# Performance work log

Hardware: AMD Instinct MI355X
Metric: run time of the kernel (lower is better)

Reference implementation:

```python
import jax, jax.numpy as jnp
import numpy as np

K = 512   # per-head dim == input dim
H = 8     # heads

def setup_inputs() -> dict:
    key = jax.random.key(0)
    ks = jax.random.split(key, 6)
    b, t = 4, 2048
    x = jax.random.normal(ks[0], (b, t, K), dtype=jnp.float32)
    s = 0.02
    Wq = jax.random.normal(ks[1], (K, K * H), dtype=jnp.float32) * s
    Wk = jax.random.normal(ks[2], (K, K * H), dtype=jnp.float32) * s
    Wv = jax.random.normal(ks[3], (K, K * H), dtype=jnp.float32) * s
    Wo = jax.random.normal(ks[4], (K * H, K), dtype=jnp.float32) * s
    bo = jnp.zeros((K,), dtype=jnp.float32)
    return {"x": x, "Wq": Wq, "Wk": Wk, "Wv": Wv, "Wo": Wo, "bo": bo}

def reference(x, Wq, Wk, Wv, Wo, bo):
    b, t, _ = x.shape
    scale = K ** 0.25
    # rearrange 'b t (k h) -> (b h) t k' == reshape (b,t,K,H) then move h next to b
    def split_heads(y):
        return y.reshape(b, t, K, H).transpose(0, 3, 1, 2)  # [b,h,t,K]
    q = split_heads(x @ Wq) / scale
    k_ = split_heads(x @ Wk) / scale
    v = split_heads(x @ Wv)
    dot = jnp.einsum('bhtk,bhsk->bhts', q, k_)      # [b,h,t,t]
    attn = jax.nn.softmax(dot, axis=-1)
    o = jnp.einsum('bhts,bhsk->bhtk', attn, v)      # [b,h,t,K]
    # '(b h) t k -> b t (h k)': heads outer in concat
    o = o.transpose(0, 2, 1, 3).reshape(b, t, H * K)
    return o @ Wo + bo
```

## Files before the change

kernel.cpp:

```cpp
#include <hip/hip_runtime.h>

typedef unsigned short u16;
typedef unsigned char u8;
typedef unsigned int u32;
typedef long i64;
typedef __attribute__((ext_vector_type(8))) short bf16x8;
typedef __attribute__((ext_vector_type(4))) float f32x4;
typedef __attribute__((ext_vector_type(16))) float f32x16;
typedef __attribute__((ext_vector_type(4))) u16 u16x4;
typedef __attribute__((ext_vector_type(4))) u32 u32x4;

__device__ __forceinline__ u16 f2bf(float f) {
  u32 u = __builtin_bit_cast(u32, f);
  return (u16)((u + 0x7FFFu + ((u >> 16) & 1u)) >> 16);
}
__device__ __forceinline__ u8 f2fp8(float f) {
  int w = __builtin_amdgcn_cvt_pk_fp8_f32(f, 0.f, 0, false);
  return (u8)(w & 0xff);
}

__device__ __forceinline__ f32x4 mfma16(bf16x8 a, bf16x8 b, f32x4 c) {
  return __builtin_amdgcn_mfma_f32_16x16x32_bf16(a, b, c, 0, 0, 0);
}
__device__ __forceinline__ f32x16 mfma32(bf16x8 a, bf16x8 b, f32x16 c) {
  return __builtin_amdgcn_mfma_f32_32x32x16_bf16(a, b, c, 0, 0, 0);
}
__device__ __forceinline__ f32x16 mfma32f8(i64 a, i64 b, f32x16 c) {
  return __builtin_amdgcn_mfma_f32_32x32x16_fp8_fp8(a, b, c, 0, 0, 0);
}

__device__ __forceinline__ void gload16(const void* g, void* l) {
  __builtin_amdgcn_global_load_lds(
      (const __attribute__((address_space(1))) unsigned int*)g,
      (__attribute__((address_space(3))) unsigned int*)l, 16, 0, 0);
}

__device__ __forceinline__ u32 cvtpk(float lo, float hi) {
  u32 r;
  asm volatile("v_cvt_pk_bf16_f32 %0, %1, %2" : "=v"(r) : "v"(lo), "v"(hi));
  return r;
}
__device__ __forceinline__ void pl32swap(u32& a, u32& b) {
  asm volatile("v_permlane32_swap_b32 %0, %1" : "+v"(a), "+v"(b));
}


__global__ void pack_x_kernel(const float* __restrict__ x, u16* __restrict__ xb) {
  const int i = blockIdx.x * 256 + threadIdx.x;
  const float4 v = ((const float4*)x)[i];
  u16x4 o;
  o[0] = f2bf(v.x); o[1] = f2bf(v.y); o[2] = f2bf(v.z); o[3] = f2bf(v.w);
  ((u16x4*)xb)[i] = o;
}

__global__ void pack_wqkv_t(const float* __restrict__ W, u16* __restrict__ Wp) {
  __shared__ u16 tile[64][72];
  const int t = threadIdx.x;
  const int c0 = blockIdx.x * 64, dd0 = blockIdx.y * 64;
#pragma unroll
  for (int s = 0; s < 4; ++s) {
    const int r = s * 16 + (t >> 4);
    const int q = (t & 15) * 4;
    const float4 v = *(const float4*)&W[(size_t)(dd0 + r) * 4096 + c0 + q];
    tile[r][q + 0] = f2bf(v.x); tile[r][q + 1] = f2bf(v.y);
    tile[r][q + 2] = f2bf(v.z); tile[r][q + 3] = f2bf(v.w);
  }
  __syncthreads();
#pragma unroll
  for (int s = 0; s < 4; ++s) {
    const int cl = s * 16 + (t >> 4);
    const int u = t & 15;
    const int cg = c0 + cl;
    const int orow = (cg & 7) * 512 + (cg >> 3);
    u16x4 o;
#pragma unroll
    for (int i = 0; i < 4; ++i) o[i] = tile[u * 4 + i][cl];
    *(u16x4*)&Wp[(size_t)orow * 512 + dd0 + u * 4] = o;
  }
}

__global__ void pack_wo_t(const float* __restrict__ W, u16* __restrict__ Wp) {
  __shared__ u16 tile[64][72];
  const int t = threadIdx.x;
  const int k0 = blockIdx.x * 64, n0 = blockIdx.y * 64;
#pragma unroll
  for (int s = 0; s < 4; ++s) {
    const int r = s * 16 + (t >> 4);
    const int q = (t & 15) * 4;
    const float4 v = *(const float4*)&W[(size_t)(k0 + r) * 512 + n0 + q];
    tile[r][q + 0] = f2bf(v.x); tile[r][q + 1] = f2bf(v.y);
    tile[r][q + 2] = f2bf(v.z); tile[r][q + 3] = f2bf(v.w);
  }
  __syncthreads();
#pragma unroll
  for (int s = 0; s < 4; ++s) {
    const int cl = s * 16 + (t >> 4);
    const int u = t & 15;
    u16x4 o;
#pragma unroll
    for (int i = 0; i < 4; ++i) o[i] = tile[u * 4 + i][cl];
    *(u16x4*)&Wp[(size_t)(n0 + cl) * 4096 + k0 + u * 4] = o;
  }
}


template <int MODE>
__global__ __launch_bounds__(256, 2) void gemm_bf16(
    const u16* __restrict__ A, const u16* __restrict__ B,
    void* __restrict__ Cout, const float* __restrict__ bias,
    int Kd, float scale) {
  __shared__ u16 Al[128 * 64];
  __shared__ u16 Bl[128 * 64];
  const int tid = threadIdx.x;
  const int lane = tid & 63;
  const int w = tid >> 6, wm = w >> 1, wn = w & 1;
  const int l15 = lane & 15, lg = lane >> 4;
  const int m0 = blockIdx.y * 128, n0 = blockIdx.x * 128;

  f32x4 acc[4][4];
  const f32x4 zero = {0.f, 0.f, 0.f, 0.f};
#pragma unroll
  for (int i = 0; i < 4; ++i)
#pragma unroll
    for (int j = 0; j < 4; ++j) acc[i][j] = zero;

  const int nk = Kd >> 6;
  for (int kt = 0; kt < nk; ++kt) {
    __syncthreads();
    const int k0 = kt << 6;
#pragma unroll
    for (int s = 0; s < 4; ++s) {
      const int chunk = s * 256 + tid;
      const int row = chunk >> 3, c = chunk & 7;
      const int cs = c ^ (row & 7);
      gload16(A + (size_t)(m0 + row) * Kd + k0 + cs * 8, &Al[chunk * 8]);
    }
#pragma unroll
    for (int s = 0; s < 4; ++s) {
      const int chunk = s * 256 + tid;
      const int row = chunk >> 3, c = chunk & 7;
      const int cs = c ^ (row & 7);
      gload16(B + (size_t)(n0 + row) * Kd + k0 + cs * 8, &Bl[chunk * 8]);
    }
    __syncthreads();
#pragma unroll
    for (int kk = 0; kk < 2; ++kk) {
      bf16x8 af[4], bfr[4];
      const int ch = kk * 4 + lg;
#pragma unroll
      for (int i = 0; i < 4; ++i) {
        const int ar = wm * 64 + i * 16 + l15;
        af[i] = *(const bf16x8*)&Al[ar * 64 + ((ch ^ (ar & 7)) * 8)];
        const int br = wn * 64 + i * 16 + l15;
        bfr[i] = *(const bf16x8*)&Bl[br * 64 + ((ch ^ (br & 7)) * 8)];
      }
#pragma unroll
      for (int i = 0; i < 4; ++i)
#pragma unroll
        for (int j = 0; j < 4; ++j)
          acc[i][j] = mfma16(af[i], bfr[j], acc[i][j]);
    }
  }

#pragma unroll
  for (int i = 0; i < 4; ++i) {
    const int gr0 = m0 + wm * 64 + i * 16 + lg * 4;
#pragma unroll
    for (int j = 0; j < 4; ++j) {
      const int gc = n0 + wn * 64 + j * 16 + l15;
      if constexpr (MODE == 0) {
        u8* O = (u8*)Cout;
        const int h = gc >> 9, d = gc & 511;
#pragma unroll
        for (int r = 0; r < 4; ++r) {
          const int grr = gr0 + r;
          const int bb = grr >> 11, t = grr & 2047;
          O[((size_t)((bb * 8 + h) * 2048 + t) << 9) + d] = f2fp8(acc[i][j][r] * scale);
        }
      } else if constexpr (MODE == 1) {
        u16* O = (u16*)Cout;
        const int h = gc >> 9, d = gc & 511;
        const int bb = gr0 >> 11, t = gr0 & 2047;
        u16x4 pk;
#pragma unroll
        for (int r = 0; r < 4; ++r) pk[r] = f2bf(acc[i][j][r]);
        *(u16x4*)&O[((size_t)((bb * 8 + h) * 512 + d) << 11) + t] = pk;
      } else if constexpr (MODE == 3) {
        u8* O = (u8*)Cout;
        const int h = gc >> 9, k = gc & 511;
#pragma unroll
        for (int r = 0; r < 4; ++r) {
          const int grr = gr0 + r;
          const int bb = grr >> 11, t = grr & 2047;
          O[((((size_t)(bb * 8 + h) * 64 + (t >> 5)) * 32 + (k >> 4)) * 32 + (t & 31)) * 16 +
            (k & 15)] = f2fp8(acc[i][j][r] * scale);
        }
      } else {
        float* O = (float*)Cout;
        const float bv = bias[gc];
#pragma unroll
        for (int r = 0; r < 4; ++r)
          O[(size_t)(gr0 + r) * 512 + gc] = acc[i][j][r] + bv;
      }
    }
  }
}


__global__ __launch_bounds__(512, 2) void attn_kernel(
    const u8* __restrict__ Qg, const u8* __restrict__ K4g,
    const u16* __restrict__ Vtg, u16* __restrict__ Og, int nbh_pxcd) {
  __shared__ u16 Vt_lds[2][512 * 32];
  __shared__ float Sxf[8][32][32];

  const int tid = threadIdx.x;
  const int lane = tid & 63;
  const int w = tid >> 6;
  const int pr = w >> 1, whalf = w & 1;
  const int l31 = lane & 31, hi = lane >> 5;

  const int bid = blockIdx.x;
  const int x8 = bid & 7, rest = bid >> 3;
  const int qt = rest & 15;
  const int bh = x8 * nbh_pxcd + (rest >> 4);

  const u8* Qb = Qg + (size_t)bh * 2048 * 512;
  const u8* K4b = K4g + (size_t)bh * 2048 * 512;
  const u16* Vb = Vtg + (size_t)bh * 2048 * 512;

  const int qrow = qt * 128 + pr * 32 + l31;
  i64 qf8[16];
  {
    const u8* qp = Qb + (size_t)qrow * 512 + whalf * 256 + hi * 8;
#pragma unroll
    for (int cc = 0; cc < 16; ++cc) qf8[cc] = *(const i64*)(qp + cc * 16);
  }

  const int koff = whalf * 16 * 512 + l31 * 16 + hi * 8;

  f32x16 acc[8];
#pragma unroll
  for (int i = 0; i < 8; ++i) acc[i] = {};
  float lsum = 0.f;

#define STAGE_V(tile, buf)                                                    \
  {                                                                           \
    _Pragma("unroll") for (int s_ = 0; s_ < 4; ++s_) {                        \
      const int chunk = s_ * 512 + tid;                                       \
      const int row = chunk >> 2, c_ = chunk & 3;                             \
      const int cs = c_ ^ ((row >> 1) & 3);                                   \
      gload16(Vb + (size_t)row * 2048 + (tile) * 32 + cs * 8,                 \
              &Vt_lds[buf][chunk * 8]);                                       \
    }                                                                         \
  }

  STAGE_V(0, 0);
  i64 kf[16];
  {
    const u8* kp = K4b + koff;
#pragma unroll
    for (int cc = 0; cc < 16; ++cc) kf[cc] = *(const i64*)(kp + cc * 512);
  }
  asm volatile("s_waitcnt vmcnt(0)" ::: "memory");
  __builtin_amdgcn_s_barrier();
  __builtin_amdgcn_sched_barrier(0);

  for (int t = 0; t < 64; ++t) {
    const int cur = t & 1;

    if (t < 63) STAGE_V(t + 1, cur ^ 1);

    f32x16 st = {};
    __builtin_amdgcn_s_setprio(1);
#pragma unroll
    for (int cc = 0; cc < 16; ++cc) st = mfma32f8(kf[cc], qf8[cc], st);
    __builtin_amdgcn_s_setprio(0);

    if (t < 63) {
      const u8* kp = K4b + ((size_t)(t + 1) << 14) + koff;
#pragma unroll
      for (int cc = 0; cc < 16; ++cc) kf[cc] = *(const i64*)(kp + cc * 512);
    }

    {
      float* sp = &Sxf[w][l31][0];
#pragma unroll
      for (int g = 0; g < 4; ++g) {
        const int slot = (2 * g + hi) ^ (l31 & 7);
        f32x4 v = {st[4 * g + 0], st[4 * g + 1], st[4 * g + 2], st[4 * g + 3]};
        *(f32x4*)&sp[slot * 4] = v;
      }
    }
    asm volatile("s_waitcnt lgkmcnt(0)" ::: "memory");
    __builtin_amdgcn_s_barrier();
    __builtin_amdgcn_sched_barrier(0);
    {
      const float* sp = &Sxf[w ^ 1][l31][0];
#pragma unroll
      for (int g = 0; g < 4; ++g) {
        const int slot = (2 * g + hi) ^ (l31 & 7);
        const f32x4 v = *(const f32x4*)&sp[slot * 4];
#pragma unroll
        for (int j = 0; j < 4; ++j) st[4 * g + j] += v[j];
      }
    }

#pragma unroll
    for (int r = 0; r < 16; ++r) {
      st[r] = __expf(st[r]);
      lsum += st[r];
    }

    bf16x8 pf0, pf1;
    {
      u32 wd[8];
#pragma unroll
      for (int g = 0; g < 4; ++g) {
        wd[2 * g] = cvtpk(st[4 * g + 0], st[4 * g + 1]);
        wd[2 * g + 1] = cvtpk(st[4 * g + 2], st[4 * g + 3]);
      }
      pl32swap(wd[0], wd[2]); pl32swap(wd[1], wd[3]);
      pl32swap(wd[4], wd[6]); pl32swap(wd[5], wd[7]);
      u32x4 f0 = {wd[0], wd[1], wd[2], wd[3]};
      u32x4 f1 = {wd[4], wd[5], wd[6], wd[7]};
      pf0 = __builtin_bit_cast(bf16x8, f0);
      pf1 = __builtin_bit_cast(bf16x8, f1);
    }

    __builtin_amdgcn_s_setprio(1);
#pragma unroll
    for (int blk = 0; blk < 8; ++blk) {
      const int drow = whalf * 256 + blk * 32 + l31;
      const int pos0 = hi ^ ((drow >> 1) & 3);
      const int pos1 = (2 + hi) ^ ((drow >> 1) & 3);
      bf16x8 v0 = *(const bf16x8*)&Vt_lds[cur][drow * 32 + pos0 * 8];
      bf16x8 v1 = *(const bf16x8*)&Vt_lds[cur][drow * 32 + pos1 * 8];
      acc[blk] = mfma32(v0, pf0, acc[blk]);
      acc[blk] = mfma32(v1, pf1, acc[blk]);
    }
    __builtin_amdgcn_s_setprio(0);

    asm volatile("s_waitcnt vmcnt(0)" ::: "memory");
    __builtin_amdgcn_s_barrier();
    __builtin_amdgcn_sched_barrier(0);
  }

  lsum += __shfl_xor(lsum, 32, 64);
  const float inv = 1.0f / lsum;
  const int bb = bh >> 3, h = bh & 7;
  const int tq = qt * 128 + pr * 32 + l31;
  u16* orow_p = Og + (size_t)(bb * 2048 + tq) * 4096 + h * 512;
#pragma unroll
  for (int blk = 0; blk < 8; ++blk) {
    const int dbase = whalf * 256 + blk * 32 + 4 * hi;
#pragma unroll
    for (int g = 0; g < 4; ++g) {
      u16x4 pk;
#pragma unroll
      for (int z = 0; z < 4; ++z) pk[z] = f2bf(acc[blk][4 * g + z] * inv);
      *(u16x4*)(orow_p + dbase + 8 * g) = pk;
    }
  }
#undef STAGE_V
}


extern "C" void kernel_launch(void* const* d_in, const int* in_sizes, int n_in,
                              void* d_out, int out_size, void* d_ws, size_t ws_size,
                              hipStream_t stream) {
  const float* x = (const float*)d_in[0];
  const float* Wq = (const float*)d_in[1];
  const float* Wk = (const float*)d_in[2];
  const float* Wv = (const float*)d_in[3];
  const float* Wo = (const float*)d_in[4];
  const float* bo = (const float*)d_in[5];
  float* out = (float*)d_out;

  const size_t MB = 1ull << 20;
  int BB;
  if (ws_size >= 216 * MB) BB = 4;
  else if (ws_size >= 120 * MB) BB = 2;
  else BB = 1;

  char* ws = (char*)d_ws;
  u16* xb  = (u16*)(ws);
  u16* Wqp = (u16*)(ws + 8 * MB);
  u16* Wkp = (u16*)(ws + 12 * MB);
  u16* Wvp = (u16*)(ws + 16 * MB);
  u16* Wot = (u16*)(ws + 20 * MB);
  u8*  Qg  = (u8*)(ws + 24 * MB);
  u8*  Kg  = (u8*)(ws + (24 + 8 * (size_t)BB) * MB);
  u16* Vtg = (u16*)(ws + (24 + 16 * (size_t)BB) * MB);
  u16* Og  = (u16*)(ws + (24 + 32 * (size_t)BB) * MB);

  pack_x_kernel<<<dim3(4096), dim3(256), 0, stream>>>(x, xb);
  pack_wqkv_t<<<dim3(64, 8), dim3(256), 0, stream>>>(Wq, Wqp);
  pack_wqkv_t<<<dim3(64, 8), dim3(256), 0, stream>>>(Wk, Wkp);
  pack_wqkv_t<<<dim3(64, 8), dim3(256), 0, stream>>>(Wv, Wvp);
  pack_wo_t<<<dim3(64, 8), dim3(256), 0, stream>>>(Wo, Wot);

  const float qk_scale = 0.21022410381342865f;

  const int nchunk = 4 / BB;
  for (int c = 0; c < nchunk; ++c) {
    const u16* Ax = xb + (size_t)c * BB * 2048 * 512;
    gemm_bf16<0><<<dim3(32, BB * 16), dim3(256), 0, stream>>>(Ax, Wqp, (void*)Qg, nullptr, 512, qk_scale);
    gemm_bf16<3><<<dim3(32, BB * 16), dim3(256), 0, stream>>>(Ax, Wkp, (void*)Kg, nullptr, 512, qk_scale);
    gemm_bf16<1><<<dim3(32, BB * 16), dim3(256), 0, stream>>>(Ax, Wvp, (void*)Vtg, nullptr, 512, 1.0f);

    attn_kernel<<<dim3(16 * BB * 8), dim3(512), 0, stream>>>(Qg, Kg, Vtg, Og, BB);

    gemm_bf16<2><<<dim3(4, BB * 16), dim3(256), 0, stream>>>(
        Og, Wot, (void*)(out + (size_t)c * BB * 2048 * 512), bo, 4096, 1.0f);
  }
}
```

Before: 582.1 us.

## Software-pipeline attention loop: lag softmax and PV by one tile, triple-buffer V

The attention main loop is skewed so that iteration t runs the QK^T MFMAs for tile t while doing the cross-wave score reduction, exp, bf16 packing and PV MFMAs for tile t-1. V tiles become triple-buffered and the score exchange buffer double-buffered, which lets each iteration use a single barrier instead of two. The setprio and sched_barrier hints are dropped. Shared memory use grows to roughly the full per-CU LDS budget, and there is an extra epilogue step plus register pressure from keeping the previous score tile live.

```diff
diff --git a/kernel.cpp b/kernel.cpp
--- a/kernel.cpp
+++ b/kernel.cpp
@@ -210,8 +210,8 @@
 __global__ __launch_bounds__(512, 2) void attn_kernel(
     const u8* __restrict__ Qg, const u8* __restrict__ K4g,
     const u16* __restrict__ Vtg, u16* __restrict__ Og, int nbh_pxcd) {
-  __shared__ u16 Vt_lds[2][512 * 32];
-  __shared__ float Sxf[8][32][32];
+  __shared__ u16 V3[3][512 * 32];
+  __shared__ float Sxf[2][8][32][32];
 
   const int tid = threadIdx.x;
   const int lane = tid & 63;
@@ -242,6 +242,7 @@
 #pragma unroll
   for (int i = 0; i < 8; ++i) acc[i] = {};
   float lsum = 0.f;
+  f32x16 sprev;
 
 #define STAGE_V(tile, buf)                                                    \
   {                                                                           \
@@ -250,7 +251,45 @@
       const int row = chunk >> 2, c_ = chunk & 3;                             \
       const int cs = c_ ^ ((row >> 1) & 3);                                   \
       gload16(Vb + (size_t)row * 2048 + (tile) * 32 + cs * 8,                 \
-              &Vt_lds[buf][chunk * 8]);                                       \
+              &V3[buf][chunk * 8]);                                           \
+    }                                                                         \
+  }
+
+#define LAGGED(p, vbuf)                                                       \
+  {                                                                           \
+    const float* sp = &Sxf[p][w ^ 1][l31][0];                                 \
+    _Pragma("unroll") for (int g = 0; g < 4; ++g) {                           \
+      const int slot = (2 * g + hi) ^ (l31 & 7);                              \
+      const f32x4 v_ = *(const f32x4*)&sp[slot * 4];                          \
+      _Pragma("unroll") for (int jj = 0; jj < 4; ++jj)                        \
+          sprev[4 * g + jj] += v_[jj];                                        \
+    }                                                                         \
+    _Pragma("unroll") for (int r = 0; r < 16; ++r) {                          \
+      sprev[r] = __expf(sprev[r]);                                            \
+      lsum += sprev[r];                                                       \
+    }                                                                         \
+    bf16x8 pf0, pf1;                                                          \
+    {                                                                         \
+      u32 wd[8];                                                              \
+      _Pragma("unroll") for (int g = 0; g < 4; ++g) {                         \
+        wd[2 * g] = cvtpk(sprev[4 * g + 0], sprev[4 * g + 1]);                \
+        wd[2 * g + 1] = cvtpk(sprev[4 * g + 2], sprev[4 * g + 3]);            \
+      }                                                                       \
+      pl32swap(wd[0], wd[2]); pl32swap(wd[1], wd[3]);                         \
+      pl32swap(wd[4], wd[6]); pl32swap(wd[5], wd[7]);                         \
+      u32x4 f0_ = {wd[0], wd[1], wd[2], wd[3]};                               \
+      u32x4 f1_ = {wd[4], wd[5], wd[6], wd[7]};                               \
+      pf0 = __builtin_bit_cast(bf16x8, f0_);                                  \
+      pf1 = __builtin_bit_cast(bf16x8, f1_);                                  \
+    }                                                                         \
+    _Pragma("unroll") for (int blk = 0; blk < 8; ++blk) {                     \
+      const int drow = whalf * 256 + blk * 32 + l31;                          \
+      const int pos0 = hi ^ ((drow >> 1) & 3);                                \
+      const int pos1 = (2 + hi) ^ ((drow >> 1) & 3);                          \
+      bf16x8 v0 = *(const bf16x8*)&V3[vbuf][drow * 32 + pos0 * 8];            \
+      bf16x8 v1 = *(const bf16x8*)&V3[vbuf][drow * 32 + pos1 * 8];            \
+      acc[blk] = mfma32(v0, pf0, acc[blk]);                                   \
+      acc[blk] = mfma32(v1, pf1, acc[blk]);                                   \
     }                                                                         \
   }
 
@@ -263,18 +302,16 @@
   }
   asm volatile("s_waitcnt vmcnt(0)" ::: "memory");
   __builtin_amdgcn_s_barrier();
-  __builtin_amdgcn_sched_barrier(0);
+
+  int vstage = 1;
+  int vread = 2;
 
   for (int t = 0; t < 64; ++t) {
-    const int cur = t & 1;
-
-    if (t < 63) STAGE_V(t + 1, cur ^ 1);
+    if (t < 63) STAGE_V(t + 1, vstage);
 
     f32x16 st = {};
-    __builtin_amdgcn_s_setprio(1);
 #pragma unroll
     for (int cc = 0; cc < 16; ++cc) st = mfma32f8(kf[cc], qf8[cc], st);
-    __builtin_amdgcn_s_setprio(0);
 
     if (t < 63) {
       const u8* kp = K4b + ((size_t)(t + 1) << 14) + koff;
@@ -283,7 +320,7 @@
     }
 
     {
-      float* sp = &Sxf[w][l31][0];
+      float* sp = &Sxf[t & 1][w][l31][0];
 #pragma unroll
       for (int g = 0; g < 4; ++g) {
         const int slot = (2 * g + hi) ^ (l31 & 7);
@@ -291,59 +328,19 @@
         *(f32x4*)&sp[slot * 4] = v;
       }
     }
-    asm volatile("s_waitcnt lgkmcnt(0)" ::: "memory");
+
+    if (t > 0) LAGGED((t - 1) & 1, vread);
+
+    sprev = st;
+
+    asm volatile("s_waitcnt vmcnt(0) lgkmcnt(0)" ::: "memory");
     __builtin_amdgcn_s_barrier();
-    __builtin_amdgcn_sched_barrier(0);
-    {
-      const float* sp = &Sxf[w ^ 1][l31][0];
-#pragma unroll
-      for (int g = 0; g < 4; ++g) {
-        const int slot = (2 * g + hi) ^ (l31 & 7);
-        const f32x4 v = *(const f32x4*)&sp[slot * 4];
-#pragma unroll
-        for (int j = 0; j < 4; ++j) st[4 * g + j] += v[j];
-      }
-    }
-
-#pragma unroll
-    for (int r = 0; r < 16; ++r) {
-      st[r] = __expf(st[r]);
-      lsum += st[r];
-    }
-
-    bf16x8 pf0, pf1;
-    {
-      u32 wd[8];
-#pragma unroll
-      for (int g = 0; g < 4; ++g) {
-        wd[2 * g] = cvtpk(st[4 * g + 0], st[4 * g + 1]);
-        wd[2 * g + 1] = cvtpk(st[4 * g + 2], st[4 * g + 3]);
-      }
-      pl32swap(wd[0], wd[2]); pl32swap(wd[1], wd[3]);
-      pl32swap(wd[4], wd[6]); pl32swap(wd[5], wd[7]);
-      u32x4 f0 = {wd[0], wd[1], wd[2], wd[3]};
-      u32x4 f1 = {wd[4], wd[5], wd[6], wd[7]};
-      pf0 = __builtin_bit_cast(bf16x8, f0);
-      pf1 = __builtin_bit_cast(bf16x8, f1);
-    }
-
-    __builtin_amdgcn_s_setprio(1);
-#pragma unroll
-    for (int blk = 0; blk < 8; ++blk) {
-      const int drow = whalf * 256 + blk * 32 + l31;
-      const int pos0 = hi ^ ((drow >> 1) & 3);
-      const int pos1 = (2 + hi) ^ ((drow >> 1) & 3);
-      bf16x8 v0 = *(const bf16x8*)&Vt_lds[cur][drow * 32 + pos0 * 8];
-      bf16x8 v1 = *(const bf16x8*)&Vt_lds[cur][drow * 32 + pos1 * 8];
-      acc[blk] = mfma32(v0, pf0, acc[blk]);
-      acc[blk] = mfma32(v1, pf1, acc[blk]);
-    }
-    __builtin_amdgcn_s_setprio(0);
-
-    asm volatile("s_waitcnt vmcnt(0)" ::: "memory");
-    __builtin_amdgcn_s_barrier();
-    __builtin_amdgcn_sched_barrier(0);
-  }
+
+    vstage = (vstage == 2) ? 0 : vstage + 1;
+    vread = (vread == 2) ? 0 : vread + 1;
+  }
+
+  LAGGED(1, vread);
 
   lsum += __shfl_xor(lsum, 32, 64);
   const float inv = 1.0f / lsum;
@@ -362,6 +359,7 @@
     }
   }
 #undef STAGE_V
+#undef LAGGED
 }
 
 
```

New measurement: 590.4 us. Within noise of the previous version (+1.4%).
